# Kernel optimization log

Measured on AMD Instinct MI355X. Metric: run time of the kernel, lower is better.

The kernel has to match this reference:

```python
import jax, jax.numpy as jnp
import numpy as np

ALPHA = 1.702
LIMIT = 7.0


def setup_inputs() -> dict:
    key = jax.random.key(0)
    ks = jax.random.split(key, 6)
    T, H, D, E = 8192, 1024, 1024, 8
    hidden_states = jax.random.normal(ks[0], (T, H), dtype=jnp.float32)
    routing_weights = jax.random.uniform(ks[1], (T, E), dtype=jnp.float32)
    # 0.02 scale keeps activations in a sane range (original uses raw randn params)
    gate_up_proj = jax.random.normal(ks[2], (E, H, 2 * D), dtype=jnp.float32) * 0.02
    gate_up_proj_bias = jax.random.normal(ks[3], (E, 2 * D), dtype=jnp.float32) * 0.02
    down_proj = jax.random.normal(ks[4], (E, D, H), dtype=jnp.float32) * 0.02
    down_proj_bias = jax.random.normal(ks[5], (E, H), dtype=jnp.float32) * 0.02
    return {
        "hidden_states": hidden_states,
        "routing_weights": routing_weights,
        "gate_up_proj": gate_up_proj,
        "gate_up_proj_bias": gate_up_proj_bias,
        "down_proj": down_proj,
        "down_proj_bias": down_proj_bias,
    }


def reference(hidden_states, routing_weights, gate_up_proj, gate_up_proj_bias,
              down_proj, down_proj_bias):
    # hidden_states: [T, H]; routing_weights: [T, E] (batch_size == T in the torch code)
    B, H = hidden_states.shape[0], hidden_states.shape[-1]
    hs = hidden_states.reshape(-1, H)  # [T, H]
    # all-experts batched GEMM: [E, T, 2D]
    gate_up = jnp.einsum('th,ehd->etd', hs, gate_up_proj) + gate_up_proj_bias[:, None, :]
    gate = jnp.minimum(gate_up[..., ::2], LIMIT)          # [E, T, D]
    up = jnp.clip(gate_up[..., 1::2], -LIMIT, LIMIT)      # [E, T, D]
    glu = gate * jax.nn.sigmoid(gate * ALPHA)
    # down projection: [E, T, H]
    next_states = jnp.einsum('etd,edh->eth', (up + 1.0) * glu, down_proj) \
        + down_proj_bias[:, None, :]
    # routing-weighted combine over experts: [T, H]
    out = jnp.einsum('eth,te->th', next_states, routing_weights)
    return out.reshape(B, -1, H)  # [T, 1, H], matching final .view(batch_size, -1, hidden)
```

## Files before the change

kernel.cpp:

```cpp
#include <hip/hip_runtime.h>
#include <hip/hip_bf16.h>

#define T_DIM 8192
#define H_DIM 1024
#define D_DIM 1024
#define E_DIM 8
#define TWO_D 2048
#define K2 8192

#define ALPHA_C 1.702f
#define LIMIT_C 7.0f

typedef __attribute__((ext_vector_type(8))) short s8v;
typedef __attribute__((ext_vector_type(4))) float f4v;

__device__ __forceinline__ void g2l16(const void* g, void* l) {
    __builtin_amdgcn_global_load_lds((const __attribute__((address_space(1))) void*)g,
                                     (__attribute__((address_space(3))) void*)l, 16, 0, 0);
}

__device__ __forceinline__ unsigned short f2bf(float f) {
    __hip_bfloat16 h = __float2bfloat16(f);
    return __builtin_bit_cast(unsigned short, h);
}


__global__ void f32_to_bf16_kernel(const float* __restrict__ in,
                                   unsigned short* __restrict__ out, size_t n) {
    size_t i = ((size_t)blockIdx.x * blockDim.x + threadIdx.x) * 4;
    if (i + 3 < n) {
        float4 v = *(const float4*)(in + i);
        ushort4 o;
        o.x = f2bf(v.x); o.y = f2bf(v.y); o.z = f2bf(v.z); o.w = f2bf(v.w);
        *(ushort4*)(out + i) = o;
    }
}

__global__ void transpose_conv_kernel(const float* __restrict__ in,
                                      unsigned short* __restrict__ out,
                                      int cols, size_t ibs, size_t obs, size_t ors,
                                      int remap) {
    __shared__ float t[32][33];
    const int b = blockIdx.z;
    const int c0 = blockIdx.x * 32, r0 = blockIdx.y * 32;
    const int tx = threadIdx.x & 31, ty = threadIdx.x >> 5;
    const float* ip = in + (size_t)b * ibs;
    #pragma unroll
    for (int i = 0; i < 4; ++i)
        t[ty + i * 8][tx] = ip[(size_t)(r0 + ty + i * 8) * cols + c0 + tx];
    __syncthreads();
    unsigned short* op = out + (size_t)b * obs;
    #pragma unroll
    for (int i = 0; i < 4; ++i) {
        int c = c0 + ty + i * 8;
        int nc = remap ? ((c & ~31) + ((c & 1) << 4) + ((c >> 1) & 15)) : c;
        op[(size_t)nc * ors + r0 + tx] = f2bf(t[tx][ty + i * 8]);
    }
}


__global__ __launch_bounds__(256, 2) void gemm1_kernel(
    const short* __restrict__ Ag0,
    const short* __restrict__ Bg0,
    const float* __restrict__ b1,
    const float* __restrict__ rw,
    __hip_bfloat16* __restrict__ act2)
{
    const int e = blockIdx.z;
    const int mBase = blockIdx.x * 128;
    const int nBase = blockIdx.y * 128;
    const int tid = threadIdx.x;
    const int lane = tid & 63;
    const int wave = tid >> 6;
    const int wm = wave >> 1, wn = wave & 1;
    const int cq = lane & 15, quad = lane >> 4;

    __shared__ __align__(16) short As[128 * 64];
    __shared__ __align__(16) short Bs[128 * 64];

    const short* Ag = Ag0 + (size_t)mBase * H_DIM;
    const short* Bg = Bg0 + ((size_t)e * TWO_D + nBase) * H_DIM;

    f4v acc[4][4];
    #pragma unroll
    for (int mt = 0; mt < 4; ++mt)
        #pragma unroll
        for (int nt = 0; nt < 4; ++nt)
            acc[mt][nt] = (f4v){0.f, 0.f, 0.f, 0.f};

    const int srow8 = lane >> 3;
    const int gco = ((lane & 7) ^ srow8) * 8;
    const int cq7 = cq & 7;

    for (int k0 = 0; k0 < H_DIM; k0 += 64) {
        #pragma unroll
        for (int i = 0; i < 4; ++i) {
            const int r = wave * 32 + i * 8 + srow8;
            g2l16(Ag + (size_t)r * H_DIM + k0 + gco, As + (wave * 32 + i * 8) * 64);
            g2l16(Bg + (size_t)r * H_DIM + k0 + gco, Bs + (wave * 32 + i * 8) * 64);
        }
        __syncthreads();
        #pragma unroll
        for (int h = 0; h < 2; ++h) {
            s8v af[4], bf[4];
            const int pc = (((h << 2) + quad) ^ cq7) * 8;
            #pragma unroll
            for (int i = 0; i < 4; ++i) {
                af[i] = *(const s8v*)(As + (wm * 64 + i * 16 + cq) * 64 + pc);
                bf[i] = *(const s8v*)(Bs + (wn * 64 + i * 16 + cq) * 64 + pc);
            }
            #pragma unroll
            for (int mt = 0; mt < 4; ++mt)
                #pragma unroll
                for (int nt = 0; nt < 4; ++nt)
                    acc[mt][nt] = __builtin_amdgcn_mfma_f32_16x16x32_bf16(
                        af[mt], bf[nt], acc[mt][nt], 0, 0, 0);
        }
        __syncthreads();
    }

    float rwv[4][4];
    #pragma unroll
    for (int mt = 0; mt < 4; ++mt)
        #pragma unroll
        for (int r = 0; r < 4; ++r)
            rwv[mt][r] = rw[(size_t)(mBase + wm * 64 + mt * 16 + quad * 4 + r) * E_DIM + e];

    #pragma unroll
    for (int p = 0; p < 2; ++p) {
        const int j = (((nBase + wn * 64 + p * 32) >> 5) << 4) + cq;
        const float gb = b1[(size_t)e * TWO_D + 2 * j];
        const float ub = b1[(size_t)e * TWO_D + 2 * j + 1];
        #pragma unroll
        for (int mt = 0; mt < 4; ++mt) {
            #pragma unroll
            for (int r = 0; r < 4; ++r) {
                float gate = acc[mt][2 * p][r] + gb;
                float up   = acc[mt][2 * p + 1][r] + ub;
                gate = fminf(gate, LIMIT_C);
                up = fminf(fmaxf(up, -LIMIT_C), LIMIT_C);
                float glu = gate / (1.f + __expf(-ALPHA_C * gate));
                float a = (up + 1.f) * glu * rwv[mt][r];
                const int row = mBase + wm * 64 + mt * 16 + quad * 4 + r;
                act2[(size_t)row * K2 + (size_t)e * D_DIM + j] = __float2bfloat16(a);
            }
        }
    }
}


__global__ __launch_bounds__(256, 2) void gemm2_kernel(
    const short* __restrict__ Ag0,
    const short* __restrict__ Bg0,
    const float* __restrict__ rw,
    const float* __restrict__ b3,
    float* __restrict__ out)
{
    const int id = blockIdx.x;
    const int nBase = (id & 7) * 128;
    const int mBase = (id >> 3) * 128;
    const int tid = threadIdx.x;
    const int lane = tid & 63;
    const int wave = tid >> 6;
    const int wm = wave >> 1, wn = wave & 1;
    const int cq = lane & 15, quad = lane >> 4;

    __shared__ __align__(16) short As[128 * 64];
    __shared__ __align__(16) short Bs[128 * 64];

    const short* Ag = Ag0 + (size_t)mBase * K2;
    const short* Bg = Bg0 + (size_t)nBase * K2;

    f4v acc[4][4];
    #pragma unroll
    for (int mt = 0; mt < 4; ++mt)
        #pragma unroll
        for (int nt = 0; nt < 4; ++nt)
            acc[mt][nt] = (f4v){0.f, 0.f, 0.f, 0.f};

    const int srow8 = lane >> 3;
    const int gco = ((lane & 7) ^ srow8) * 8;
    const int cq7 = cq & 7;

    for (int k0 = 0; k0 < K2; k0 += 64) {
        #pragma unroll
        for (int i = 0; i < 4; ++i) {
            const int r = wave * 32 + i * 8 + srow8;
            g2l16(Ag + (size_t)r * K2 + k0 + gco, As + (wave * 32 + i * 8) * 64);
            g2l16(Bg + (size_t)r * K2 + k0 + gco, Bs + (wave * 32 + i * 8) * 64);
        }
        __syncthreads();
        #pragma unroll
        for (int h = 0; h < 2; ++h) {
            s8v af[4], bf[4];
            const int pc = (((h << 2) + quad) ^ cq7) * 8;
            #pragma unroll
            for (int i = 0; i < 4; ++i) {
                af[i] = *(const s8v*)(As + (wm * 64 + i * 16 + cq) * 64 + pc);
                bf[i] = *(const s8v*)(Bs + (wn * 64 + i * 16 + cq) * 64 + pc);
            }
            #pragma unroll
            for (int mt = 0; mt < 4; ++mt)
                #pragma unroll
                for (int nt = 0; nt < 4; ++nt)
                    acc[mt][nt] = __builtin_amdgcn_mfma_f32_16x16x32_bf16(
                        af[mt], bf[nt], acc[mt][nt], 0, 0, 0);
        }
        __syncthreads();
    }

    #pragma unroll
    for (int mt = 0; mt < 4; ++mt) {
        #pragma unroll
        for (int r = 0; r < 4; ++r) {
            const int row = mBase + wm * 64 + mt * 16 + quad * 4 + r;
            const float4 rwa = *(const float4*)(rw + (size_t)row * E_DIM);
            const float4 rwb = *(const float4*)(rw + (size_t)row * E_DIM + 4);
            #pragma unroll
            for (int nt = 0; nt < 4; ++nt) {
                const int col = nBase + wn * 64 + nt * 16 + cq;
                float bias = rwa.x * b3[0 * H_DIM + col] + rwa.y * b3[1 * H_DIM + col]
                           + rwa.z * b3[2 * H_DIM + col] + rwa.w * b3[3 * H_DIM + col]
                           + rwb.x * b3[4 * H_DIM + col] + rwb.y * b3[5 * H_DIM + col]
                           + rwb.z * b3[6 * H_DIM + col] + rwb.w * b3[7 * H_DIM + col];
                out[(size_t)row * H_DIM + col] = acc[mt][nt][r] + bias;
            }
        }
    }
}


extern "C" void kernel_launch(void* const* d_in, const int* in_sizes, int n_in,
                              void* d_out, int out_size, void* d_ws, size_t ws_size,
                              hipStream_t stream) {
    const float* hs = (const float*)d_in[0];
    const float* rw = (const float*)d_in[1];
    const float* w1 = (const float*)d_in[2];
    const float* b1 = (const float*)d_in[3];
    const float* w3 = (const float*)d_in[4];
    const float* b3 = (const float*)d_in[5];
    float* out = (float*)d_out;

    char* ws = (char*)d_ws;
    unsigned short* hsb  = (unsigned short*)(ws);
    unsigned short* w1b  = (unsigned short*)(ws + ((size_t)16 << 20));
    unsigned short* w3b  = (unsigned short*)(ws + ((size_t)48 << 20));
    unsigned short* act2 = (unsigned short*)(ws + ((size_t)64 << 20));

    {
        size_t n = (size_t)T_DIM * H_DIM;
        f32_to_bf16_kernel<<<dim3(n / (256 * 4)), dim3(256), 0, stream>>>(hs, hsb, n);
    }
    transpose_conv_kernel<<<dim3(TWO_D / 32, H_DIM / 32, E_DIM), dim3(256), 0, stream>>>(
        w1, w1b, TWO_D, (size_t)H_DIM * TWO_D, (size_t)TWO_D * H_DIM, (size_t)H_DIM, 1);
    transpose_conv_kernel<<<dim3(H_DIM / 32, D_DIM / 32, E_DIM), dim3(256), 0, stream>>>(
        w3, w3b, H_DIM, (size_t)D_DIM * H_DIM, (size_t)D_DIM, (size_t)K2, 0);
    gemm1_kernel<<<dim3(T_DIM / 128, TWO_D / 128, E_DIM), dim3(256), 0, stream>>>(
        (const short*)hsb, (const short*)w1b, b1, rw, (__hip_bfloat16*)act2);
    gemm2_kernel<<<dim3(512), dim3(256), 0, stream>>>(
        (const short*)act2, (const short*)w3b, rw, b3, out);
}
```

Baseline: 607.2 us.

## Double-buffer LDS tiles in gemm2 to overlap global loads with MFMA

The down-projection GEMM kernel now uses two LDS buffers for A and B. It prefetches the next K tile with global_load_lds while MFMAs run on the current tile, and raises wave priority around the compute section. Each iteration needs only one barrier instead of two, and memory latency is meant to be hidden behind compute. LDS use doubles to 64KB per block, which may lower occupancy below the two blocks per CU requested in the launch bounds.

```diff
diff --git a/kernel.cpp b/kernel.cpp
--- a/kernel.cpp
+++ b/kernel.cpp
@@ -149,6 +149,10 @@
 }
 
 
+#define FEN asm volatile("" ::: "memory")
+#define BARR { FEN; __builtin_amdgcn_s_barrier(); FEN; }
+#define VMW0 asm volatile("s_waitcnt vmcnt(0)" ::: "memory")
+
 __global__ __launch_bounds__(256, 2) void gemm2_kernel(
     const short* __restrict__ Ag0,
     const short* __restrict__ Bg0,
@@ -165,8 +169,8 @@
     const int wm = wave >> 1, wn = wave & 1;
     const int cq = lane & 15, quad = lane >> 4;
 
-    __shared__ __align__(16) short As[128 * 64];
-    __shared__ __align__(16) short Bs[128 * 64];
+    __shared__ __align__(16) short As[2][128 * 64];
+    __shared__ __align__(16) short Bs[2][128 * 64];
 
     const short* Ag = Ag0 + (size_t)mBase * K2;
     const short* Bg = Bg0 + (size_t)nBase * K2;
@@ -182,22 +186,40 @@
     const int gco = ((lane & 7) ^ srow8) * 8;
     const int cq7 = cq & 7;
 
+    #pragma unroll
+    for (int i = 0; i < 4; ++i) {
+        const int r = wave * 32 + i * 8 + srow8;
+        g2l16(Ag + (size_t)r * K2 + 0 + gco, &As[0][(wave * 32 + i * 8) * 64]);
+        g2l16(Bg + (size_t)r * K2 + 0 + gco, &Bs[0][(wave * 32 + i * 8) * 64]);
+    }
+    VMW0;
+    BARR;
+
+    int cur = 0;
+    #pragma unroll 1
     for (int k0 = 0; k0 < K2; k0 += 64) {
-        #pragma unroll
-        for (int i = 0; i < 4; ++i) {
-            const int r = wave * 32 + i * 8 + srow8;
-            g2l16(Ag + (size_t)r * K2 + k0 + gco, As + (wave * 32 + i * 8) * 64);
-            g2l16(Bg + (size_t)r * K2 + k0 + gco, Bs + (wave * 32 + i * 8) * 64);
-        }
-        __syncthreads();
+        if (k0 + 64 < K2) {
+            #pragma unroll
+            for (int i = 0; i < 4; ++i) {
+                const int r = wave * 32 + i * 8 + srow8;
+                g2l16(Ag + (size_t)r * K2 + k0 + 64 + gco,
+                      &As[cur ^ 1][(wave * 32 + i * 8) * 64]);
+                g2l16(Bg + (size_t)r * K2 + k0 + 64 + gco,
+                      &Bs[cur ^ 1][(wave * 32 + i * 8) * 64]);
+            }
+        }
+        FEN;
+        const short* Ab = As[cur];
+        const short* Bb = Bs[cur];
+        __builtin_amdgcn_s_setprio(1);
         #pragma unroll
         for (int h = 0; h < 2; ++h) {
             s8v af[4], bf[4];
             const int pc = (((h << 2) + quad) ^ cq7) * 8;
             #pragma unroll
             for (int i = 0; i < 4; ++i) {
-                af[i] = *(const s8v*)(As + (wm * 64 + i * 16 + cq) * 64 + pc);
-                bf[i] = *(const s8v*)(Bs + (wn * 64 + i * 16 + cq) * 64 + pc);
+                af[i] = *(const s8v*)(Ab + (wm * 64 + i * 16 + cq) * 64 + pc);
+                bf[i] = *(const s8v*)(Bb + (wn * 64 + i * 16 + cq) * 64 + pc);
             }
             #pragma unroll
             for (int mt = 0; mt < 4; ++mt)
@@ -206,7 +228,10 @@
                     acc[mt][nt] = __builtin_amdgcn_mfma_f32_16x16x32_bf16(
                         af[mt], bf[nt], acc[mt][nt], 0, 0, 0);
         }
-        __syncthreads();
+        __builtin_amdgcn_s_setprio(0);
+        VMW0;
+        BARR;
+        cur ^= 1;
     }
 
     #pragma unroll
```

Result: no change. 606.8 us (-0.1%).
